# Kernel optimization log

Hardware: AMD Instinct MI355X
Metric: run time of the kernel (lower is better)

The kernel has to match this reference:

```python
import jax, jax.numpy as jnp
import numpy as np

BATCH = 4096
DIM = 128
TEMP = 0.5

def setup_inputs() -> dict:
    key = jax.random.key(0)
    k1, k2 = jax.random.split(key)
    proj_1 = jax.random.normal(k1, (BATCH, DIM), dtype=jnp.float32)
    proj_2 = jax.random.normal(k2, (BATCH, DIM), dtype=jnp.float32)
    return {"proj_1": proj_1, "proj_2": proj_2}

def _l2norm(x, eps=1e-12):
    # matches F.normalize(p=2, dim=1)
    n = jnp.sqrt(jnp.sum(x * x, axis=1, keepdims=True))
    return x / jnp.maximum(n, eps)

def reference(proj_1, proj_2):
    B = proj_1.shape[0]
    z_i = _l2norm(proj_1)
    z_j = _l2norm(proj_2)
    reps = jnp.concatenate([z_i, z_j], axis=0)          # [2B, D]
    # cosine similarity of normalized vectors == dot product; (2B,D)x(D,2B) matmul
    sim = reps @ reps.T                                 # [2B, 2B]
    sim_ij = jnp.einsum('bd,bd->b', z_i, z_j)           # diag(sim, +B)
    sim_ji = sim_ij                                     # diag(sim, -B) is symmetric
    positives = jnp.concatenate([sim_ij, sim_ji], axis=0)  # [2B]
    nominator = jnp.exp(positives / TEMP)
    mask = (~jnp.eye(2 * B, dtype=bool)).astype(sim.dtype)
    denominator = jnp.sum(mask * jnp.exp(sim / TEMP), axis=1)  # [2B]
    all_losses = -jnp.log(nominator / denominator)
    loss = jnp.sum(all_losses) / (2 * B)
    return loss
```

## Files before the change

kernel.cpp:

```cpp
#include <hip/hip_runtime.h>
#include <hip/hip_bf16.h>
#include <math.h>

#define BATCH 4096
#define DIM 128
#define TWO_B 8192
#define SCALE 1.69864374f

typedef float floatx4 __attribute__((ext_vector_type(4)));
typedef int   intx4  __attribute__((ext_vector_type(4)));
typedef long  longx2 __attribute__((ext_vector_type(2)));

__device__ __forceinline__ longx2 as_l2(intx4 v) {
    union { intx4 a; longx2 b; } u; u.a = v; return u.b;
}
__device__ __forceinline__ unsigned char to_fp8(float v) {
    return (unsigned char)(__builtin_amdgcn_cvt_pk_fp8_f32(v, v, 0, false) & 0xff);
}


__global__ __launch_bounds__(256) void norm_kernel(const float* __restrict__ p1,
                                                   const float* __restrict__ p2,
                                                   unsigned char* __restrict__ repsF,
                                                   float* __restrict__ pos,
                                                   float* __restrict__ out) {
    int tid = threadIdx.x;
    int w = tid >> 6, l = tid & 63;
    int b = blockIdx.x * 4 + w;
    const float* r1 = p1 + (size_t)b * DIM;
    const float* r2 = p2 + (size_t)b * DIM;
    float x0 = r1[l], x1 = r1[l + 64];
    float y0 = r2[l], y1 = r2[l + 64];
    float s1 = x0 * x0 + x1 * x1;
    float s2 = y0 * y0 + y1 * y1;
    float s12 = x0 * y0 + x1 * y1;
    #pragma unroll
    for (int off = 32; off; off >>= 1) {
        s1  += __shfl_xor(s1, off);
        s2  += __shfl_xor(s2, off);
        s12 += __shfl_xor(s12, off);
    }
    float n1 = fmaxf(sqrtf(s1), 1e-12f);
    float n2 = fmaxf(sqrtf(s2), 1e-12f);
    float i1 = SCALE / n1;
    float i2 = SCALE / n2;

    int r1i = b, r2i = b + BATCH;
    int off0 = ((l >> 5) & 1) * 8 + ((l >> 3) & 3) * 256 + (l & 7);
    size_t a1 = (size_t)(r1i >> 4) * 2048 + (r1i & 15) * 16 + off0;
    size_t a2 = (size_t)(r2i >> 4) * 2048 + (r2i & 15) * 16 + off0;
    repsF[a1]        = to_fp8(x0 * i1);
    repsF[a1 + 1024] = to_fp8(x1 * i1);
    repsF[a2]        = to_fp8(y0 * i2);
    repsF[a2 + 1024] = to_fp8(y1 * i2);

    if (l == 0) {
        pos[b] = s12 / (n1 * n2);
        if (b == 0) out[0] = 0.0f;
    }
}

__global__ __launch_bounds__(256, 4) void sim_kernel(const unsigned char* __restrict__ repsF,
                                                     float* __restrict__ part) {
    __shared__ float lds[4][16][68];
    int tid = threadIdx.x;
    int wid = tid >> 6, lane = tid & 63;
    int wm = wid >> 1, wn = wid & 1;
    int lr = lane & 15, q = lane >> 4;
    int r = blockIdx.y;
    int c = blockIdx.x;
    int TM, TN;
    if (c < 64 - r) { TM = r;      TN = r + c; }
    else            { TM = 63 - r; TN = TM + (c - (64 - r)); }
    if (TM == TN && wm == 1 && wn == 0) return;
    int tm = 2 * TM + wm, tn = 2 * TN + wn;
    bool diag = (tm == tn);

    const char* base = (const char*)repsF;
    int lofs = q * 256 + lr * 16;
    const char* ab = base + tm * 8192 + lofs;
    const char* bb = base + tn * 8192 + lofs;

    longx2 aF[4][2], bF[4][2];
    #pragma unroll
    for (int mi = 0; mi < 4; ++mi)
        #pragma unroll
        for (int h = 0; h < 2; ++h) {
            aF[mi][h] = as_l2(*(const intx4*)(ab + mi * 2048 + h * 1024));
            bF[mi][h] = as_l2(*(const intx4*)(bb + mi * 2048 + h * 1024));
        }

    float cs[4] = {0.0f, 0.0f, 0.0f, 0.0f};
    floatx4 rpacc[4];

    #pragma unroll
    for (int p = 0; p < 2; ++p) {
        floatx4 acc[4][2] = {};
        #pragma unroll
        for (int ck = 0; ck < 4; ++ck) {
            int h = ck >> 1, sel = ck & 1;
            #pragma unroll
            for (int mi = 0; mi < 4; ++mi)
                #pragma unroll
                for (int nn = 0; nn < 2; ++nn)
                    acc[mi][nn] = __builtin_amdgcn_mfma_f32_16x16x32_fp8_fp8(
                        aF[mi][h][sel], bF[2 * p + nn][h][sel], acc[mi][nn], 0, 0, 0);
        }
        #pragma unroll
        for (int mi = 0; mi < 4; ++mi) {
            #pragma unroll
            for (int reg = 0; reg < 4; ++reg) {
                float e0 = __builtin_amdgcn_exp2f(acc[mi][0][reg]);
                float e1 = __builtin_amdgcn_exp2f(acc[mi][1][reg]);
                if (diag && (q * 4 + reg) == lr) {
                    if (mi == 2 * p)     e0 = 0.0f;
                    if (mi == 2 * p + 1) e1 = 0.0f;
                }
                cs[2 * p]     += e0;
                cs[2 * p + 1] += e1;
                float rsum = e0 + e1;
                rpacc[mi][reg] = (p == 0) ? rsum : (rpacc[mi][reg] + rsum);
            }
        }
    }

    float* myl = &lds[wid][0][0];
    #pragma unroll
    for (int mi = 0; mi < 4; ++mi)
        *(floatx4*)&myl[lr * 68 + mi * 16 + q * 4] = rpacc[mi];
    asm volatile("s_waitcnt lgkmcnt(0)" ::: "memory");
    {
        float rs = 0.0f;
        #pragma unroll
        for (int j = 0; j < 16; ++j)
            rs += myl[j * 68 + lane];
        part[(size_t)tn * TWO_B + tm * 64 + lane] = rs;
    }
    if (!diag) {
        #pragma unroll
        for (int ni = 0; ni < 4; ++ni) {
            cs[ni] += __shfl_xor(cs[ni], 16);
            cs[ni] += __shfl_xor(cs[ni], 32);
        }
        if (q == 0) {
            #pragma unroll
            for (int ni = 0; ni < 4; ++ni)
                part[(size_t)tm * TWO_B + tn * 64 + ni * 16 + lr] = cs[ni];
        }
    }
}

__global__ __launch_bounds__(256) void reduce_kernel(const float* __restrict__ part,
                                                     const float* __restrict__ pos,
                                                     float* __restrict__ out) {
    __shared__ float stage[4][64];
    int tid = threadIdx.x;
    int w = tid >> 6, l = tid & 63;
    int rr = blockIdx.x * 64 + l;
    const float* p = part + (size_t)(w * 32) * TWO_B + rr;
    float s0 = 0.0f, s1 = 0.0f, s2 = 0.0f, s3 = 0.0f;
    #pragma unroll
    for (int k = 0; k < 32; k += 4) {
        s0 += p[(size_t)(k + 0) * TWO_B];
        s1 += p[(size_t)(k + 1) * TWO_B];
        s2 += p[(size_t)(k + 2) * TWO_B];
        s3 += p[(size_t)(k + 3) * TWO_B];
    }
    stage[w][l] = (s0 + s1) + (s2 + s3);
    __syncthreads();
    if (w == 0) {
        float s = (stage[0][l] + stage[1][l]) + (stage[2][l] + stage[3][l]);
        float v = __logf(s) - 2.0f * pos[rr & (BATCH - 1)];
        #pragma unroll
        for (int off = 32; off; off >>= 1) v += __shfl_xor(v, off);
        if (l == 0) atomicAdd(out, v * (1.0f / TWO_B));
    }
}

extern "C" void kernel_launch(void* const* d_in, const int* in_sizes, int n_in,
                              void* d_out, int out_size, void* d_ws, size_t ws_size,
                              hipStream_t stream) {
    const float* p1 = (const float*)d_in[0];
    const float* p2 = (const float*)d_in[1];
    float* out = (float*)d_out;

    char* ws = (char*)d_ws;
    unsigned char* repsF = (unsigned char*)ws;
    float* pos  = (float*)(ws + (size_t)TWO_B * DIM);
    float* part = pos + BATCH;

    norm_kernel<<<BATCH / 4, 256, 0, stream>>>(p1, p2, repsF, pos, out);
    sim_kernel<<<dim3(65, 32), 256, 0, stream>>>(repsF, part);
    reduce_kernel<<<TWO_B / 64, 256, 0, stream>>>(part, pos, out);
}
```

Before: 73.16 us.

## Fuse reduction into sim kernel via atomic row sums and last-block finalize

Result: slower. 106.3 us (+45.2%).

```diff
diff --git a/kernel.cpp b/kernel.cpp
--- a/kernel.cpp
+++ b/kernel.cpp
@@ -5,6 +5,7 @@
 #define BATCH 4096
 #define DIM 128
 #define TWO_B 8192
+#define NBLOCKS 2080
 #define SCALE 1.69864374f
 
 typedef float floatx4 __attribute__((ext_vector_type(4)));
@@ -23,7 +24,8 @@
                                                    const float* __restrict__ p2,
                                                    unsigned char* __restrict__ repsF,
                                                    float* __restrict__ pos,
-                                                   float* __restrict__ out) {
+                                                   float* __restrict__ denom,
+                                                   int* __restrict__ counter) {
     int tid = threadIdx.x;
     int w = tid >> 6, l = tid & 63;
     int b = blockIdx.x * 4 + w;
@@ -54,15 +56,19 @@
     repsF[a2]        = to_fp8(y0 * i2);
     repsF[a2 + 1024] = to_fp8(y1 * i2);
 
-    if (l == 0) {
-        pos[b] = s12 / (n1 * n2);
-        if (b == 0) out[0] = 0.0f;
-    }
+    if (l == 0) pos[b] = s12 / (n1 * n2);
+    if (blockIdx.x < 32) denom[blockIdx.x * 256 + tid] = 0.0f;
+    if (blockIdx.x == 32 && tid == 0) *counter = 0;
 }
 
 __global__ __launch_bounds__(256, 4) void sim_kernel(const unsigned char* __restrict__ repsF,
-                                                     float* __restrict__ part) {
+                                                     float* __restrict__ denom,
+                                                     const float* __restrict__ pos,
+                                                     int* __restrict__ counter,
+                                                     float* __restrict__ out) {
     __shared__ float lds[4][16][68];
+    __shared__ int lastFlag;
+    __shared__ float sred[4];
     int tid = threadIdx.x;
     int wid = tid >> 6, lane = tid & 63;
     int wm = wid >> 1, wn = wid & 1;
@@ -72,109 +78,113 @@
     int TM, TN;
     if (c < 64 - r) { TM = r;      TN = r + c; }
     else            { TM = 63 - r; TN = TM + (c - (64 - r)); }
-    if (TM == TN && wm == 1 && wn == 0) return;
+    bool skip = (TM == TN) && (wm == 1) && (wn == 0);
     int tm = 2 * TM + wm, tn = 2 * TN + wn;
     bool diag = (tm == tn);
 
-    const char* base = (const char*)repsF;
-    int lofs = q * 256 + lr * 16;
-    const char* ab = base + tm * 8192 + lofs;
-    const char* bb = base + tn * 8192 + lofs;
-
-    longx2 aF[4][2], bF[4][2];
+    if (!skip) {
+        const char* base = (const char*)repsF;
+        int lofs = q * 256 + lr * 16;
+        const char* ab = base + tm * 8192 + lofs;
+        const char* bb = base + tn * 8192 + lofs;
+
+        longx2 aF[4][2], bF[4][2];
+        #pragma unroll
+        for (int mi = 0; mi < 4; ++mi)
+            #pragma unroll
+            for (int h = 0; h < 2; ++h) {
+                aF[mi][h] = as_l2(*(const intx4*)(ab + mi * 2048 + h * 1024));
+                bF[mi][h] = as_l2(*(const intx4*)(bb + mi * 2048 + h * 1024));
+            }
+
+        float cs[4] = {0.0f, 0.0f, 0.0f, 0.0f};
+        floatx4 rpacc[4];
+
+        #pragma unroll
+        for (int p = 0; p < 2; ++p) {
+            floatx4 acc[4][2] = {};
+            #pragma unroll
+            for (int ck = 0; ck < 4; ++ck) {
+                int h = ck >> 1, sel = ck & 1;
+                #pragma unroll
+                for (int mi = 0; mi < 4; ++mi)
+                    #pragma unroll
+                    for (int nn = 0; nn < 2; ++nn)
+                        acc[mi][nn] = __builtin_amdgcn_mfma_f32_16x16x32_fp8_fp8(
+                            aF[mi][h][sel], bF[2 * p + nn][h][sel], acc[mi][nn], 0, 0, 0);
+            }
+            #pragma unroll
+            for (int mi = 0; mi < 4; ++mi) {
+                #pragma unroll
+                for (int reg = 0; reg < 4; ++reg) {
+                    float e0 = __builtin_amdgcn_exp2f(acc[mi][0][reg]);
+                    float e1 = __builtin_amdgcn_exp2f(acc[mi][1][reg]);
+                    if (diag && (q * 4 + reg) == lr) {
+                        if (mi == 2 * p)     e0 = 0.0f;
+                        if (mi == 2 * p + 1) e1 = 0.0f;
+                    }
+                    cs[2 * p]     += e0;
+                    cs[2 * p + 1] += e1;
+                    float rsum = e0 + e1;
+                    rpacc[mi][reg] = (p == 0) ? rsum : (rpacc[mi][reg] + rsum);
+                }
+            }
+        }
+
+        float* myl = &lds[wid][0][0];
+        #pragma unroll
+        for (int mi = 0; mi < 4; ++mi)
+            *(floatx4*)&myl[lr * 68 + mi * 16 + q * 4] = rpacc[mi];
+        asm volatile("s_waitcnt lgkmcnt(0)" ::: "memory");
+        {
+            float rs = 0.0f;
+            #pragma unroll
+            for (int j = 0; j < 16; ++j)
+                rs += myl[j * 68 + lane];
+            atomicAdd(&denom[tm * 64 + lane], rs);
+        }
+        if (!diag) {
+            #pragma unroll
+            for (int ni = 0; ni < 4; ++ni) {
+                cs[ni] += __shfl_xor(cs[ni], 16);
+                cs[ni] += __shfl_xor(cs[ni], 32);
+            }
+            if (q == 0) {
+                #pragma unroll
+                for (int ni = 0; ni < 4; ++ni)
+                    atomicAdd(&denom[tn * 64 + ni * 16 + lr], cs[ni]);
+            }
+        }
+    }
+
+    __syncthreads();
+    if (tid == 0) {
+        int old = __hip_atomic_fetch_add(counter, 1, __ATOMIC_ACQ_REL,
+                                         __HIP_MEMORY_SCOPE_AGENT);
+        lastFlag = (old == NBLOCKS - 1);
+    }
+    __syncthreads();
+    if (!lastFlag) return;
+
+    float a0 = 0.0f, a1 = 0.0f, a2 = 0.0f, a3 = 0.0f;
+    #pragma unroll 1
+    for (int rr = tid; rr < TWO_B; rr += 1024) {
+        float d0 = __hip_atomic_load(&denom[rr],       __ATOMIC_RELAXED, __HIP_MEMORY_SCOPE_AGENT);
+        float d1 = __hip_atomic_load(&denom[rr + 256], __ATOMIC_RELAXED, __HIP_MEMORY_SCOPE_AGENT);
+        float d2 = __hip_atomic_load(&denom[rr + 512], __ATOMIC_RELAXED, __HIP_MEMORY_SCOPE_AGENT);
+        float d3 = __hip_atomic_load(&denom[rr + 768], __ATOMIC_RELAXED, __HIP_MEMORY_SCOPE_AGENT);
+        a0 += __logf(d0) - 2.0f * pos[rr & (BATCH - 1)];
+        a1 += __logf(d1) - 2.0f * pos[(rr + 256) & (BATCH - 1)];
+        a2 += __logf(d2) - 2.0f * pos[(rr + 512) & (BATCH - 1)];
+        a3 += __logf(d3) - 2.0f * pos[(rr + 768) & (BATCH - 1)];
+    }
+    float v = (a0 + a1) + (a2 + a3);
     #pragma unroll
-    for (int mi = 0; mi < 4; ++mi)
-        #pragma unroll
-        for (int h = 0; h < 2; ++h) {
-            aF[mi][h] = as_l2(*(const intx4*)(ab + mi * 2048 + h * 1024));
-            bF[mi][h] = as_l2(*(const intx4*)(bb + mi * 2048 + h * 1024));
-        }
-
-    float cs[4] = {0.0f, 0.0f, 0.0f, 0.0f};
-    floatx4 rpacc[4];
-
-    #pragma unroll
-    for (int p = 0; p < 2; ++p) {
-        floatx4 acc[4][2] = {};
-        #pragma unroll
-        for (int ck = 0; ck < 4; ++ck) {
-            int h = ck >> 1, sel = ck & 1;
-            #pragma unroll
-            for (int mi = 0; mi < 4; ++mi)
-                #pragma unroll
-                for (int nn = 0; nn < 2; ++nn)
-                    acc[mi][nn] = __builtin_amdgcn_mfma_f32_16x16x32_fp8_fp8(
-                        aF[mi][h][sel], bF[2 * p + nn][h][sel], acc[mi][nn], 0, 0, 0);
-        }
-        #pragma unroll
-        for (int mi = 0; mi < 4; ++mi) {
-            #pragma unroll
-            for (int reg = 0; reg < 4; ++reg) {
-                float e0 = __builtin_amdgcn_exp2f(acc[mi][0][reg]);
-                float e1 = __builtin_amdgcn_exp2f(acc[mi][1][reg]);
-                if (diag && (q * 4 + reg) == lr) {
-                    if (mi == 2 * p)     e0 = 0.0f;
-                    if (mi == 2 * p + 1) e1 = 0.0f;
-                }
-                cs[2 * p]     += e0;
-                cs[2 * p + 1] += e1;
-                float rsum = e0 + e1;
-                rpacc[mi][reg] = (p == 0) ? rsum : (rpacc[mi][reg] + rsum);
-            }
-        }
-    }
-
-    float* myl = &lds[wid][0][0];
-    #pragma unroll
-    for (int mi = 0; mi < 4; ++mi)
-        *(floatx4*)&myl[lr * 68 + mi * 16 + q * 4] = rpacc[mi];
-    asm volatile("s_waitcnt lgkmcnt(0)" ::: "memory");
-    {
-        float rs = 0.0f;
-        #pragma unroll
-        for (int j = 0; j < 16; ++j)
-            rs += myl[j * 68 + lane];
-        part[(size_t)tn * TWO_B + tm * 64 + lane] = rs;
-    }
-    if (!diag) {
-        #pragma unroll
-        for (int ni = 0; ni < 4; ++ni) {
-            cs[ni] += __shfl_xor(cs[ni], 16);
-            cs[ni] += __shfl_xor(cs[ni], 32);
-        }
-        if (q == 0) {
-            #pragma unroll
-            for (int ni = 0; ni < 4; ++ni)
-                part[(size_t)tm * TWO_B + tn * 64 + ni * 16 + lr] = cs[ni];
-        }
-    }
-}
-
-__global__ __launch_bounds__(256) void reduce_kernel(const float* __restrict__ part,
-                                                     const float* __restrict__ pos,
-                                                     float* __restrict__ out) {
-    __shared__ float stage[4][64];
-    int tid = threadIdx.x;
-    int w = tid >> 6, l = tid & 63;
-    int rr = blockIdx.x * 64 + l;
-    const float* p = part + (size_t)(w * 32) * TWO_B + rr;
-    float s0 = 0.0f, s1 = 0.0f, s2 = 0.0f, s3 = 0.0f;
-    #pragma unroll
-    for (int k = 0; k < 32; k += 4) {
-        s0 += p[(size_t)(k + 0) * TWO_B];
-        s1 += p[(size_t)(k + 1) * TWO_B];
-        s2 += p[(size_t)(k + 2) * TWO_B];
-        s3 += p[(size_t)(k + 3) * TWO_B];
-    }
-    stage[w][l] = (s0 + s1) + (s2 + s3);
+    for (int off = 32; off; off >>= 1) v += __shfl_xor(v, off);
+    if (lane == 0) sred[wid] = v;
     __syncthreads();
-    if (w == 0) {
-        float s = (stage[0][l] + stage[1][l]) + (stage[2][l] + stage[3][l]);
-        float v = __logf(s) - 2.0f * pos[rr & (BATCH - 1)];
-        #pragma unroll
-        for (int off = 32; off; off >>= 1) v += __shfl_xor(v, off);
-        if (l == 0) atomicAdd(out, v * (1.0f / TWO_B));
-    }
+    if (tid == 0)
+        out[0] = ((sred[0] + sred[1]) + (sred[2] + sred[3])) * (1.0f / TWO_B);
 }
 
 extern "C" void kernel_launch(void* const* d_in, const int* in_sizes, int n_in,
@@ -186,10 +196,10 @@
 
     char* ws = (char*)d_ws;
     unsigned char* repsF = (unsigned char*)ws;
-    float* pos  = (float*)(ws + (size_t)TWO_B * DIM);
-    float* part = pos + BATCH;
-
-    norm_kernel<<<BATCH / 4, 256, 0, stream>>>(p1, p2, repsF, pos, out);
-    sim_kernel<<<dim3(65, 32), 256, 0, stream>>>(repsF, part);
-    reduce_kernel<<<TWO_B / 64, 256, 0, stream>>>(part, pos, out);
-}
+    float* pos   = (float*)(ws + (size_t)TWO_B * DIM);
+    float* denom = pos + BATCH;
+    int* counter = (int*)(denom + TWO_B);
+
+    norm_kernel<<<BATCH / 4, 256, 0, stream>>>(p1, p2, repsF, pos, denom, counter);
+    sim_kernel<<<dim3(65, 32), 256, 0, stream>>>(repsF, denom, pos, counter, out);
+}
```
